# Kernel tuning notes

Hardware: AMD Instinct MI355X
Metric: run time of the kernel (lower is better)

## Reference

```python
import jax, jax.numpy as jnp
import numpy as np

BLOCK = (4, 4, 4)
NUM_HEADS = 8


def setup_inputs() -> dict:
    key = jax.random.key(0)
    ks = jax.random.split(key, 5)
    C = 128
    return {
        "x": jax.random.normal(ks[0], (2, C, 32, 62, 62), dtype=jnp.float32),
        "qkv_w": jax.random.normal(ks[1], (3 * C, C), dtype=jnp.float32) * 0.02,
        "qkv_b": jax.random.normal(ks[2], (3 * C,), dtype=jnp.float32) * 0.02,
        "conv_w": jax.random.normal(ks[3], (C, C, 1, 1, 1), dtype=jnp.float32) * 0.02,
        "conv_b": jax.random.normal(ks[4], (C,), dtype=jnp.float32) * 0.02,
    }


def reference(x, qkv_w, qkv_b, conv_w, conv_b):
    b0, b1, b2 = BLOCK
    heads = NUM_HEADS
    B, C, D, H0, W0 = x.shape
    pad_r = (-W0) % b2
    pad_b = (-H0) % b1
    x = jnp.pad(x, ((0, 0), (0, 0), (0, 0), (0, pad_b), (0, pad_r)))
    H, W = H0 + pad_b, W0 + pad_r
    d, h, w = D // b0, H // b1, W // b2
    hd = C // heads
    scale = hd ** (-0.5)
    T = b0 * b1 * b2  # tokens per 3D window
    nw = d * h * w    # number of windows

    # partition into windows: (B, nw, T, C)
    xw = x.reshape(B, C, d, b0, h, b1, w, b2).transpose(0, 2, 4, 6, 3, 5, 7, 1)
    xw = xw.reshape(B, nw, T, C)

    qkv = xw @ qkv_w.T + qkv_b  # (B, nw, T, 3C)
    qkv = qkv.reshape(B, nw, T, 3, heads, hd).transpose(3, 0, 1, 4, 2, 5)
    q, k, v = qkv[0], qkv[1], qkv[2]  # (B, nw, heads, T, hd)

    attn = jnp.einsum('bnhtc,bnhsc->bnhts', q, k) * scale

    if pad_r > 0 or pad_b > 0:
        mask = jnp.zeros((H, W), dtype=attn.dtype)
        if pad_b > 0:
            mask = mask.at[-pad_b:, :].set(1.0)
        if pad_r > 0:
            mask = mask.at[:, -pad_r:].set(1.0)
        # (h*w, b1*b2) per-2D-window pad flags
        mask = mask.reshape(h, b1, w, b2).transpose(0, 2, 1, 3).reshape(h * w, b1 * b2)
        am = mask[:, None, :] - mask[:, :, None]  # (h*w, b1*b2, b1*b2)
        am = jnp.where(am != 0, jnp.asarray(-1000.0, attn.dtype), jnp.asarray(0.0, attn.dtype))
        # tile over depth windows and depth tokens (matches torch .repeat)
        am = jnp.tile(am, (d, b0, b0))  # (nw, T, T)
        attn = attn + am[None, :, None, :, :]

    attn = jax.nn.softmax(attn, axis=-1)
    o = jnp.einsum('bnhts,bnhsc->bnhtc', attn, v)  # (B, nw, heads, T, hd)

    o = o.reshape(B, d, h, w, heads, b0, b1, b2, hd)
    o = o.transpose(0, 4, 8, 1, 5, 2, 6, 3, 7).reshape(B, C, D, H, W)
    o = o[:, :, :, :H0, :W0]

    # 1x1x1 Conv3d == channel mixing
    out = jnp.einsum('bcdhw,oc->bodhw', o, conv_w[:, :, 0, 0, 0])
    out = out + conv_b[None, :, None, None, None]
    return out
```

## Files before the change

kernel.cpp:

```cpp
#include <hip/hip_runtime.h>

typedef _Float16 f16x8 __attribute__((ext_vector_type(8)));
typedef _Float16 f16x4 __attribute__((ext_vector_type(4)));
typedef __fp16   fp16x2 __attribute__((ext_vector_type(2)));
typedef float    f32x4 __attribute__((ext_vector_type(4)));
typedef unsigned int u32x2 __attribute__((ext_vector_type(2)));

__device__ __forceinline__ f32x4 mfma32(f16x8 a, f16x8 b, f32x4 c) {
  return __builtin_amdgcn_mfma_f32_16x16x32_f16(a, b, c, 0, 0, 0);
}
__device__ __forceinline__ f32x4 mfma16(f16x4 a, f16x4 b, f32x4 c) {
#if __has_builtin(__builtin_amdgcn_mfma_f32_16x16x16f16)
  return __builtin_amdgcn_mfma_f32_16x16x16f16(a, b, c, 0, 0, 0);
#else
  f32x4 d;
  asm volatile("v_mfma_f32_16x16x16_f16 %0, %1, %2, %3"
               : "=v"(d) : "v"(a), "v"(b), "v"(c));
  return d;
#endif
}

__device__ __forceinline__ unsigned pk2(float a, float b) {
  union { fp16x2 h; unsigned u; } cv;
  cv.h = __builtin_amdgcn_cvt_pkrtz(a, b);
  return cv.u;
}

#define TR_READ(dst, addr, OFF) \
  asm volatile("ds_read_b64_tr_b16 %0, %1 offset:" OFF \
               : "=v"(dst) : "v"(addr) : "memory")

__global__ void cvt_weights(const float* __restrict__ qw, const float* __restrict__ cw,
                            _Float16* __restrict__ wq, _Float16* __restrict__ wc) {
  const int i = blockIdx.x * 256 + threadIdx.x;
  if (i < 384 * 128) wq[i] = (_Float16)qw[i];
  if (i < 128 * 128) wc[i] = (_Float16)cw[i];
}

__global__ void __launch_bounds__(512, 4)
win_attn(const float* __restrict__ xg, const _Float16* __restrict__ wq,
         const float* __restrict__ qbias, const _Float16* __restrict__ wc,
         const float* __restrict__ cb, float* __restrict__ outg)
{
  __shared__ char xsm[2][16384];
  __shared__ char wsm[8][4096];

  const int tid  = threadIdx.x;
  const int lane = tid & 63;
  const int wv   = tid >> 6;
  const int l15  = lane & 15;
  const int g    = lane >> 4;

  const int raw = blockIdx.x;
  const int wp  = ((raw & 7) << 8) | (raw >> 3);
  const int wid0 = wp * 2;
  const int ww0 = wid0 & 15, hh = (wid0 >> 4) & 15, dd = (wid0 >> 8) & 7, bb = wid0 >> 11;
  const int ww1 = ww0 + 1;

  unsigned long long pm0 = 0ull, pm1 = 0ull;
  if (hh == 15)  { pm0 |= 0xFF00FF00FF00FF00ull; pm1 |= 0xFF00FF00FF00FF00ull; }
  if (ww1 == 15)   pm1 |= 0xCCCCCCCCCCCCCCCCull;

  const f32x4 fz = {0.f, 0.f, 0.f, 0.f};
  const float LOG2E = 1.4426950408889634f;
  const int swzA = l15 << 4;
  const int vswz = (l15 & 7) << 4;

  char* sb = wsm[wv];
  const unsigned sb32 = (unsigned)(unsigned long long)sb;
  const unsigned trb  = sb32 + 8u * (unsigned)lane;

  const int m4 = lane & 3, q4 = lane >> 2;
  const int i0 = q4 >> 2, i1 = q4 & 3;
  const int z = dd * 4 + i0, y = hh * 4 + i1;
  const bool yv = (y < 62);

  auto stage_loads = [&](int wwl, float (&va)[4][4]) {
    const bool full = (wwl < 15);
#pragma unroll
    for (int it = 0; it < 4; ++it) {
      const int c = wv * 16 + it * 4 + m4;
      const float* src = xg + (((size_t)(bb * 128 + c) * 32 + (size_t)z) * 3844
                               + (size_t)(y * 62 + wwl * 4));
      float a0 = 0.f, a1 = 0.f, a2 = 0.f, a3 = 0.f;
      if (yv) {
        const float2 lo = *reinterpret_cast<const float2*>(src);
        a0 = lo.x; a1 = lo.y;
        if (full) {
          const float2 hi = *reinterpret_cast<const float2*>(src + 2);
          a2 = hi.x; a3 = hi.y;
        }
      }
      va[it][0] = a0; va[it][1] = a1; va[it][2] = a2; va[it][3] = a3;
    }
  };
  auto stage_write = [&](char* xb, float (&va)[4][4]) {
#pragma unroll
    for (int it = 0; it < 4; ++it) {
      float v0 = va[it][0], v1 = va[it][1], v2 = va[it][2], v3 = va[it][3];
      float t0 = __shfl_xor((m4 & 1) ? v0 : v1, 1);
      float t1 = __shfl_xor((m4 & 1) ? v2 : v3, 1);
      if (m4 & 1) { v0 = t0; v2 = t1; } else { v1 = t0; v3 = t1; }
      float t2 = __shfl_xor((m4 & 2) ? v0 : v2, 2);
      float t3 = __shfl_xor((m4 & 2) ? v1 : v3, 2);
      if (m4 & 2) { v0 = t2; v1 = t3; } else { v2 = t2; v3 = t3; }
      f16x4 pk; pk[0] = (_Float16)v0; pk[1] = (_Float16)v1;
                pk[2] = (_Float16)v2; pk[3] = (_Float16)v3;
      const int c0 = wv * 16 + it * 4;
      *reinterpret_cast<f16x4*>(xb + ((lane * 256 + 2 * c0) ^ ((lane & 15) << 4))) = pk;
    }
  };

  auto qkv_attn = [&](const char* xb, unsigned long long pm, unsigned (&opk)[4][2]) {
    f16x8 av0, av1;
#pragma unroll
    for (int co = 0; co < 3; ++co) {
      f32x4 acc[4] = {fz, fz, fz, fz};
      const int col = co * 128 + wv * 16 + l15;
      __builtin_amdgcn_s_setprio(1);
#pragma unroll
      for (int kk = 0; kk < 4; ++kk) {
        const f16x8 bfr = *reinterpret_cast<const f16x8*>(wq + col * 128 + kk * 32 + g * 8);
#pragma unroll
        for (int ri = 0; ri < 4; ++ri) {
          const f16x8 a = *reinterpret_cast<const f16x8*>(
              xb + (ri * 16 + l15) * 256 + ((kk * 64 + g * 16) ^ swzA));
          acc[ri] = mfma32(a, bfr, acc[ri]);
        }
      }
      __builtin_amdgcn_s_setprio(0);
      const float bias = qbias[col];

      if (co == 2) {
        unsigned vp[4][2];
#pragma unroll
        for (int ri = 0; ri < 4; ++ri) {
          vp[ri][0] = pk2(acc[ri][0] + bias, acc[ri][1] + bias);
          vp[ri][1] = pk2(acc[ri][2] + bias, acc[ri][3] + bias);
        }
        const int srcA = l15 + 32 * (g & 1);
        const bool hi = (g >= 2);
        {
          const unsigned a0 = __shfl(vp[0][0], srcA);
          const unsigned a1 = __shfl(vp[0][1], srcA);
          const unsigned a2 = __shfl(vp[0][0], srcA + 16);
          const unsigned a3 = __shfl(vp[0][1], srcA + 16);
          const unsigned b0 = __shfl(vp[1][0], srcA);
          const unsigned b1 = __shfl(vp[1][1], srcA);
          const unsigned b2 = __shfl(vp[1][0], srcA + 16);
          const unsigned b3 = __shfl(vp[1][1], srcA + 16);
          union { unsigned w[4]; f16x8 v; } u;
          u.w[0] = hi ? b0 : a0; u.w[1] = hi ? b1 : a1;
          u.w[2] = hi ? b2 : a2; u.w[3] = hi ? b3 : a3;
          av0 = u.v;
        }
        {
          const unsigned a0 = __shfl(vp[2][0], srcA);
          const unsigned a1 = __shfl(vp[2][1], srcA);
          const unsigned a2 = __shfl(vp[2][0], srcA + 16);
          const unsigned a3 = __shfl(vp[2][1], srcA + 16);
          const unsigned b0 = __shfl(vp[3][0], srcA);
          const unsigned b1 = __shfl(vp[3][1], srcA);
          const unsigned b2 = __shfl(vp[3][0], srcA + 16);
          const unsigned b3 = __shfl(vp[3][1], srcA + 16);
          union { unsigned w[4]; f16x8 v; } u;
          u.w[0] = hi ? b0 : a0; u.w[1] = hi ? b1 : a1;
          u.w[2] = hi ? b2 : a2; u.w[3] = hi ? b3 : a3;
          av1 = u.v;
        }
      } else {
        const int base = (co == 0) ? 2048 : 0;
        const float sc = (co == 0) ? 0.25f : 1.0f;
#pragma unroll
        for (int ri = 0; ri < 4; ++ri) {
          const int off = ri * 512 + l15 * 32 + g * 8;
          u32x2 w;
          w[0] = pk2((acc[ri][0] + bias) * sc, (acc[ri][1] + bias) * sc);
          w[1] = pk2((acc[ri][2] + bias) * sc, (acc[ri][3] + bias) * sc);
          *reinterpret_cast<u32x2*>(sb + base + off) = w;
        }
      }
    }
    asm volatile("s_waitcnt lgkmcnt(0)" ::: "memory");

    f16x4 ka[4], qa[4];
    TR_READ(ka[0], trb, "0");
    TR_READ(ka[1], trb, "512");
    TR_READ(ka[2], trb, "1024");
    TR_READ(ka[3], trb, "1536");
    TR_READ(qa[0], trb, "2048");
    TR_READ(qa[1], trb, "2560");
    TR_READ(qa[2], trb, "3072");
    TR_READ(qa[3], trb, "3584");
    asm volatile("s_waitcnt lgkmcnt(0)" ::: "memory");
    __builtin_amdgcn_sched_barrier(0);

#pragma unroll
    for (int tjp = 0; tjp < 2; ++tjp) {
      const int tj0 = 2 * tjp, tj1 = 2 * tjp + 1;
      f32x4 st2[4][2];
#pragma unroll
      for (int si = 0; si < 4; ++si) {
        st2[si][0] = mfma16(ka[si], qa[tj0], fz);
        st2[si][1] = mfma16(ka[si], qa[tj1], fz);
      }

      if (pm) {
#pragma unroll
        for (int tjc = 0; tjc < 2; ++tjc) {
          const int t = (2 * tjp + tjc) * 16 + l15;
          const unsigned ft = (unsigned)(pm >> t) & 1u;
#pragma unroll
          for (int si = 0; si < 4; ++si)
#pragma unroll
            for (int r = 0; r < 4; ++r) {
              const int s = si * 16 + g * 4 + r;
              const unsigned fs = (unsigned)(pm >> s) & 1u;
              if (fs != ft) st2[si][tjc][r] -= 1000.f;
            }
        }
      }

#pragma unroll
      for (int tjc = 0; tjc < 2; ++tjc) {
        float mx = st2[0][tjc][0];
#pragma unroll
        for (int si = 0; si < 4; ++si)
#pragma unroll
          for (int r = 0; r < 4; ++r) mx = fmaxf(mx, st2[si][tjc][r]);
        mx = fmaxf(mx, __shfl_xor(mx, 16));
        mx = fmaxf(mx, __shfl_xor(mx, 32));
        float sum = 0.f;
#pragma unroll
        for (int si = 0; si < 4; ++si)
#pragma unroll
          for (int r = 0; r < 4; ++r) {
            const float e = __builtin_amdgcn_exp2f((st2[si][tjc][r] - mx) * LOG2E);
            st2[si][tjc][r] = e; sum += e;
          }
        sum += __shfl_xor(sum, 16);
        sum += __shfl_xor(sum, 32);
        const float inv = __builtin_amdgcn_rcpf(sum);
#pragma unroll
        for (int si = 0; si < 4; ++si)
#pragma unroll
          for (int r = 0; r < 4; ++r) st2[si][tjc][r] *= inv;
      }

#pragma unroll
      for (int tjc = 0; tjc < 2; ++tjc) {
        const int tl = tjc * 16 + l15;
#pragma unroll
        for (int si = 0; si < 4; ++si) {
          u32x2 w;
          w[0] = pk2(st2[si][tjc][0], st2[si][tjc][1]);
          w[1] = pk2(st2[si][tjc][2], st2[si][tjc][3]);
          *reinterpret_cast<u32x2*>(sb + tl * 128 + ((si * 32 + g * 8) ^ vswz)) = w;
        }
      }
      asm volatile("s_waitcnt lgkmcnt(0)" ::: "memory");

      f32x4 oa0 = fz, oa1 = fz;
      {
        const f16x8 pa00 = *reinterpret_cast<const f16x8*>(
            sb + l15 * 128 + ((g * 16) ^ vswz));
        const f16x8 pa10 = *reinterpret_cast<const f16x8*>(
            sb + (16 + l15) * 128 + ((g * 16) ^ vswz));
        __builtin_amdgcn_s_setprio(1);
        oa0 = mfma32(av0, pa00, oa0);
        oa1 = mfma32(av0, pa10, oa1);
        const f16x8 pa01 = *reinterpret_cast<const f16x8*>(
            sb + l15 * 128 + ((64 + g * 16) ^ vswz));
        const f16x8 pa11 = *reinterpret_cast<const f16x8*>(
            sb + (16 + l15) * 128 + ((64 + g * 16) ^ vswz));
        oa0 = mfma32(av1, pa01, oa0);
        oa1 = mfma32(av1, pa11, oa1);
        __builtin_amdgcn_s_setprio(0);
      }

      if (tjp == 0) {
        opk[0][0] = pk2(oa0[0], oa0[1]); opk[0][1] = pk2(oa0[2], oa0[3]);
        opk[1][0] = pk2(oa1[0], oa1[1]); opk[1][1] = pk2(oa1[2], oa1[3]);
      } else {
        opk[2][0] = pk2(oa0[0], oa0[1]); opk[2][1] = pk2(oa0[2], oa0[3]);
        opk[3][0] = pk2(oa1[0], oa1[1]); opk[3][1] = pk2(oa1[2], oa1[3]);
      }
      __builtin_amdgcn_sched_barrier(0);
    }
  };

  auto write_o = [&](char* xb, unsigned (&opk)[4][2]) {
#pragma unroll
    for (int tj = 0; tj < 4; ++tj) {
      const int t = tj * 16 + l15;
      u32x2 w0; w0[0] = opk[tj][0]; w0[1] = opk[tj][1];
      *reinterpret_cast<u32x2*>(xb + t * 256 + ((wv * 32 + g * 8) ^ ((t & 15) << 4))) = w0;
    }
  };

  auto conv_store = [&](const char* xb, int wwl) {
    f32x4 cacc[4] = {fz, fz, fz, fz};
    const int cout = wv * 16 + l15;
    __builtin_amdgcn_s_setprio(1);
#pragma unroll
    for (int kk = 0; kk < 4; ++kk) {
      const f16x8 bfr = *reinterpret_cast<const f16x8*>(wc + cout * 128 + kk * 32 + g * 8);
#pragma unroll
      for (int ri = 0; ri < 4; ++ri) {
        const f16x8 a = *reinterpret_cast<const f16x8*>(
            xb + (ri * 16 + l15) * 256 + ((kk * 64 + g * 16) ^ swzA));
        cacc[ri] = mfma32(a, bfr, cacc[ri]);
      }
    }
    __builtin_amdgcn_s_setprio(0);
    const int yy = hh * 4 + g;
    if (yy < 62) {
      const float bias = cb[cout];
#pragma unroll
      for (int ri = 0; ri < 4; ++ri) {
        const int zz = dd * 4 + ri;
        float* dst = outg + (((size_t)(bb * 128 + cout) * 32 + (size_t)zz) * 3844
                             + (size_t)(yy * 62 + wwl * 4));
        float2 lo; lo.x = cacc[ri][0] + bias; lo.y = cacc[ri][1] + bias;
        *reinterpret_cast<float2*>(dst) = lo;
        if (wwl < 15) {
          float2 hi; hi.x = cacc[ri][2] + bias; hi.y = cacc[ri][3] + bias;
          *reinterpret_cast<float2*>(dst + 2) = hi;
        }
      }
    }
  };

  float va[4][4];
  stage_loads(ww0, va);
  stage_write(xsm[0], va);
  __syncthreads();

  unsigned opk[4][2];
  qkv_attn(xsm[0], pm0, opk);
  stage_loads(ww1, va);
  __syncthreads();
  write_o(xsm[0], opk);
  stage_write(xsm[1], va);
  __syncthreads();

  conv_store(xsm[0], ww0);
  qkv_attn(xsm[1], pm1, opk);
  __syncthreads();
  write_o(xsm[1], opk);
  __syncthreads();
  conv_store(xsm[1], ww1);
}

extern "C" void kernel_launch(void* const* d_in, const int* in_sizes, int n_in,
                              void* d_out, int out_size, void* d_ws, size_t ws_size,
                              hipStream_t stream) {
  const float* x  = (const float*)d_in[0];
  const float* qw = (const float*)d_in[1];
  const float* qb = (const float*)d_in[2];
  const float* cw = (const float*)d_in[3];
  const float* cb = (const float*)d_in[4];
  float* out = (float*)d_out;

  if (ws_size < (size_t)(384 * 128 + 128 * 128) * sizeof(_Float16)) return;
  _Float16* wq = (_Float16*)d_ws;
  _Float16* wc = wq + 384 * 128;

  cvt_weights<<<192, 256, 0, stream>>>(qw, cw, wq, wc);
  win_attn<<<2048, 512, 0, stream>>>(x, wq, qb, wc, cb, out);
}
```

Before: 174.8 us.

## Stage V through LDS and issue next-window loads before attention compute

The per-wave V fragment is no longer rearranged with sixteen cross-lane shuffles. It is written to a swizzled region of the wave's shared-memory scratch and read back as f16x8 vectors, and the scratch grows to make room. The QKV/attention lambda is split in two so the global loads for the second window are issued after the QKV projection but before the attention math, hiding their latency. The cost is more LDS per block, which may reduce occupancy, and more live registers across the split.

```diff
diff --git a/kernel.cpp b/kernel.cpp
--- a/kernel.cpp
+++ b/kernel.cpp
@@ -43,7 +43,7 @@
          const float* __restrict__ cb, float* __restrict__ outg)
 {
   __shared__ char xsm[2][16384];
-  __shared__ char wsm[8][4096];
+  __shared__ char wsm[8][6144];
 
   const int tid  = threadIdx.x;
   const int lane = tid & 63;
@@ -111,8 +111,8 @@
     }
   };
 
-  auto qkv_attn = [&](const char* xb, unsigned long long pm, unsigned (&opk)[4][2]) {
-    f16x8 av0, av1;
+  auto qkv_part1 = [&](const char* xb, f16x4 (&ka)[4], f16x4 (&qa)[4],
+                       f16x8& av0, f16x8& av1) {
 #pragma unroll
     for (int co = 0; co < 3; ++co) {
       f32x4 acc[4] = {fz, fz, fz, fz};
@@ -132,41 +132,13 @@
       const float bias = qbias[col];
 
       if (co == 2) {
-        unsigned vp[4][2];
 #pragma unroll
         for (int ri = 0; ri < 4; ++ri) {
-          vp[ri][0] = pk2(acc[ri][0] + bias, acc[ri][1] + bias);
-          vp[ri][1] = pk2(acc[ri][2] + bias, acc[ri][3] + bias);
-        }
-        const int srcA = l15 + 32 * (g & 1);
-        const bool hi = (g >= 2);
-        {
-          const unsigned a0 = __shfl(vp[0][0], srcA);
-          const unsigned a1 = __shfl(vp[0][1], srcA);
-          const unsigned a2 = __shfl(vp[0][0], srcA + 16);
-          const unsigned a3 = __shfl(vp[0][1], srcA + 16);
-          const unsigned b0 = __shfl(vp[1][0], srcA);
-          const unsigned b1 = __shfl(vp[1][1], srcA);
-          const unsigned b2 = __shfl(vp[1][0], srcA + 16);
-          const unsigned b3 = __shfl(vp[1][1], srcA + 16);
-          union { unsigned w[4]; f16x8 v; } u;
-          u.w[0] = hi ? b0 : a0; u.w[1] = hi ? b1 : a1;
-          u.w[2] = hi ? b2 : a2; u.w[3] = hi ? b3 : a3;
-          av0 = u.v;
-        }
-        {
-          const unsigned a0 = __shfl(vp[2][0], srcA);
-          const unsigned a1 = __shfl(vp[2][1], srcA);
-          const unsigned a2 = __shfl(vp[2][0], srcA + 16);
-          const unsigned a3 = __shfl(vp[2][1], srcA + 16);
-          const unsigned b0 = __shfl(vp[3][0], srcA);
-          const unsigned b1 = __shfl(vp[3][1], srcA);
-          const unsigned b2 = __shfl(vp[3][0], srcA + 16);
-          const unsigned b3 = __shfl(vp[3][1], srcA + 16);
-          union { unsigned w[4]; f16x8 v; } u;
-          u.w[0] = hi ? b0 : a0; u.w[1] = hi ? b1 : a1;
-          u.w[2] = hi ? b2 : a2; u.w[3] = hi ? b3 : a3;
-          av1 = u.v;
+          const int s0 = ri * 16 + g * 4;
+          *reinterpret_cast<unsigned*>(sb + 4096 + l15 * 128 + ((2 * s0) ^ vswz))
+              = pk2(acc[ri][0] + bias, acc[ri][1] + bias);
+          *reinterpret_cast<unsigned*>(sb + 4096 + l15 * 128 + ((2 * (s0 + 2)) ^ vswz))
+              = pk2(acc[ri][2] + bias, acc[ri][3] + bias);
         }
       } else {
         const int base = (co == 0) ? 2048 : 0;
@@ -183,7 +155,6 @@
     }
     asm volatile("s_waitcnt lgkmcnt(0)" ::: "memory");
 
-    f16x4 ka[4], qa[4];
     TR_READ(ka[0], trb, "0");
     TR_READ(ka[1], trb, "512");
     TR_READ(ka[2], trb, "1024");
@@ -192,9 +163,14 @@
     TR_READ(qa[1], trb, "2560");
     TR_READ(qa[2], trb, "3072");
     TR_READ(qa[3], trb, "3584");
+    av0 = *reinterpret_cast<const f16x8*>(sb + 4096 + l15 * 128 + ((g * 16) ^ vswz));
+    av1 = *reinterpret_cast<const f16x8*>(sb + 4096 + l15 * 128 + ((64 + g * 16) ^ vswz));
     asm volatile("s_waitcnt lgkmcnt(0)" ::: "memory");
     __builtin_amdgcn_sched_barrier(0);
-
+  };
+
+  auto attn_chunks = [&](unsigned long long pm, f16x4 (&ka)[4], f16x4 (&qa)[4],
+                         f16x8 av0, f16x8 av1, unsigned (&opk)[4][2]) {
 #pragma unroll
     for (int tjp = 0; tjp < 2; ++tjp) {
       const int tj0 = 2 * tjp, tj1 = 2 * tjp + 1;
@@ -331,21 +307,26 @@
     }
   };
 
+  f16x4 ka[4], qa[4];
+  f16x8 av0, av1;
   float va[4][4];
+  unsigned opk[4][2];
+
   stage_loads(ww0, va);
   stage_write(xsm[0], va);
   __syncthreads();
 
-  unsigned opk[4][2];
-  qkv_attn(xsm[0], pm0, opk);
+  qkv_part1(xsm[0], ka, qa, av0, av1);
   stage_loads(ww1, va);
+  attn_chunks(pm0, ka, qa, av0, av1, opk);
   __syncthreads();
   write_o(xsm[0], opk);
   stage_write(xsm[1], va);
   __syncthreads();
 
   conv_store(xsm[0], ww0);
-  qkv_attn(xsm[1], pm1, opk);
+  qkv_part1(xsm[1], ka, qa, av0, av1);
+  attn_chunks(pm1, ka, qa, av0, av1, opk);
   __syncthreads();
   write_o(xsm[1], opk);
   __syncthreads();
```

Measured after the change: 172.7 us. About the same (-1.2%).
